# Kernel optimization log

Hardware: AMD Instinct MI355X
Metric: run time of the kernel (lower is better)

Reference implementation:

```python
import jax, jax.numpy as jnp
import numpy as np


def _hippo_dplr(n):
    # HiPPO-LegS -> NPLR -> DPLR (diagonal plus low rank) init, as in S4
    pr = np.sqrt(1.0 + 2.0 * np.arange(n))
    A = -(np.tril(pr[:, None] * pr[None, :]) - np.diag(np.arange(n)))
    p = np.sqrt(np.arange(n) + 0.5)
    b = np.sqrt(2.0 * np.arange(n) + 1.0)
    S = A + p[:, None] * p[None, :]
    lam_re = np.full(n, np.mean(np.diagonal(S)))
    lam_im, V = np.linalg.eigh(S * -1j)  # S*-1j is Hermitian
    p_c = V.conj().T @ p.astype(np.complex128)
    b_c = V.conj().T @ b.astype(np.complex128)
    return lam_re, lam_im, p_c, b_c


def setup_inputs():
    B, L, H, N = 4, 1024, 512, 64
    key = jax.random.key(0)
    kx, kc, ks, k1, k2 = jax.random.split(key, 5)
    lam_re, lam_im, p_c, b_c = _hippo_dplr(N)
    c = jax.random.normal(kc, (N, 2)) * (0.5 ** 0.5)
    f32 = lambda a: jnp.asarray(a, dtype=jnp.float32)
    return {
        'x': jax.random.normal(kx, (B, L, H), dtype=jnp.float32),
        'norm_weight': jnp.ones((H,), jnp.float32),
        'norm_bias': jnp.zeros((H,), jnp.float32),
        'lambda_re': f32(lam_re), 'lambda_im': f32(lam_im),
        'p_re': f32(p_c.real), 'p_im': f32(p_c.imag),
        'b_re': f32(b_c.real), 'b_im': f32(b_c.imag),
        'c_re': c[:, 0].astype(jnp.float32), 'c_im': c[:, 1].astype(jnp.float32),
        'd': jnp.ones((), jnp.float32),
        'log_step': jax.random.uniform(ks, (), jnp.float32, float(np.log(0.001)), float(np.log(0.1))),
        'out_w': (jax.random.normal(k1, (H, H), jnp.float32) / np.sqrt(H)).astype(jnp.float32),
        'out_b': jnp.zeros((H,), jnp.float32),
        'out2_w': (jax.random.normal(k2, (H, H), jnp.float32) / np.sqrt(H)).astype(jnp.float32),
        'out2_b': jnp.zeros((H,), jnp.float32),
    }


def reference(x, norm_weight, norm_bias, lambda_re, lambda_im, p_re, p_im,
              b_re, b_im, c_re, c_im, d, log_step, out_w, out_b, out2_w, out2_b):
    Bsz, L, H = x.shape
    skip = x
    # LayerNorm over channel dim (eps=1e-5, eqx default)
    mu = jnp.mean(x, -1, keepdims=True)
    var = jnp.mean((x - mu) ** 2, -1, keepdims=True)
    xn = (x - mu) / jnp.sqrt(var + 1e-5) * norm_weight + norm_bias
    # --- S4 DPLR bilinear discretization ---
    lam = (lambda_re + 1j * lambda_im).astype(jnp.complex64)
    p = (p_re + 1j * p_im).astype(jnp.complex64)
    b = (b_re + 1j * b_im).astype(jnp.complex64)
    c = (c_re + 1j * c_im).astype(jnp.complex64)
    step = jnp.exp(log_step).astype(jnp.complex64)
    N = lam.shape[0]
    I = jnp.eye(N, dtype=jnp.complex64)
    A = jnp.diag(lam) - p[:, None] * p[None, :].conj()
    A0 = (2.0 / step) * I + A
    Dinv = jnp.diag(1.0 / ((2.0 / step) - lam))
    qcD = p.conj()[None, :] @ Dinv           # [1,N]
    Dp = Dinv @ p[:, None]                   # [N,1]
    A1 = Dinv - (Dp @ qcD) / (1.0 + (qcD @ p[:, None]))  # Woodbury
    Ab = A1 @ A0                             # [N,N] discrete state matrix
    Bb = 2.0 * (A1 @ b[:, None])[:, 0]       # [N]
    # --- sequential state-space scan over time, vectorized over (B,H) lanes ---
    u = xn.astype(jnp.complex64)             # [B,L,H]

    def step_fn(state, u_t):                 # state: [B,H,N], u_t: [B,H]
        new = jnp.einsum('nm,bhm->bhn', Ab, state) + u_t[..., None] * Bb
        return new, jnp.einsum('n,bhn->bh', c, new).real

    init = jnp.zeros((Bsz, H, N), jnp.complex64)
    _, ys = jax.lax.scan(step_fn, init, jnp.moveaxis(u, 1, 0))  # ys: [L,B,H]
    y = jnp.moveaxis(ys, 0, 1) + d * xn      # feedthrough term
    # --- GELU + GLU-style gated output projection, residual ---
    y = jax.nn.gelu(y)
    gate = jax.nn.sigmoid(y @ out2_w.T + out2_b)
    return skip + (y @ out_w.T + out_b) * gate
```

## Files before the change

kernel.cpp:

```cpp
#include <hip/hip_runtime.h>
#include <math.h>

#define HDIM 512
#define LSEQ 1024
#define BSZ  4

typedef __attribute__((ext_vector_type(8))) short short8;
typedef __attribute__((ext_vector_type(4))) float floatx4;
typedef _Float16 half8 __attribute__((ext_vector_type(8)));

__device__ __forceinline__ float2 cmul(float2 a, float2 b) {
  float2 r;
  r.x = a.x * b.x - a.y * b.y;
  r.y = a.x * b.y + a.y * b.x;
  return r;
}
__device__ __forceinline__ float2 cadd(float2 a, float2 b) {
  float2 r; r.x = a.x + b.x; r.y = a.y + b.y; return r;
}
__device__ __forceinline__ float2 cfma(float2 a, float2 b, float2 c) {
  c.x += a.x * b.x - a.y * b.y;
  c.y += a.x * b.y + a.y * b.x;
  return c;
}
__device__ __forceinline__ ushort f2h(float f) {
  _Float16 h = (_Float16)f;
  return *(ushort*)&h;
}
__device__ __forceinline__ uint pack2h(float a, float b) {
  return (uint)f2h(a) | ((uint)f2h(b) << 16);
}

template<int CTRL, int RM>
__device__ __forceinline__ float dpp_add(float v) {
  int x = __builtin_amdgcn_update_dpp(0, __float_as_int(v), CTRL, RM, 0xF, false);
  return v + __int_as_float(x);
}
__device__ __forceinline__ float red8(float v) {
  v = dpp_add<0xB1, 0xF>(v);
  v = dpp_add<0x4E, 0xF>(v);
  v = dpp_add<0x141, 0xF>(v);
  return v;
}
__device__ __forceinline__ float red64(float v) {
  v = dpp_add<0x121, 0xF>(v);
  v = dpp_add<0x122, 0xF>(v);
  v = dpp_add<0x124, 0xF>(v);
  v = dpp_add<0x128, 0xF>(v);
  v = dpp_add<0x142, 0xA>(v);
  v = dpp_add<0x143, 0xC>(v);
  return __int_as_float(__builtin_amdgcn_readlane(__float_as_int(v), 63));
}

__global__ __launch_bounds__(576) void stage1_kernel(
    const float* __restrict__ x, const float* __restrict__ nw,
    const float* __restrict__ nb, ushort* __restrict__ xn16,
    const float* __restrict__ lre, const float* __restrict__ lim,
    const float* __restrict__ pre, const float* __restrict__ pim,
    const float* __restrict__ bre, const float* __restrict__ bim,
    const float* __restrict__ cre, const float* __restrict__ cim,
    const float* __restrict__ logstep, float* __restrict__ Kout,
    const float* __restrict__ w1, const float* __restrict__ w2,
    ushort* __restrict__ Wst) {
  __shared__ float2 Ldab[64], Lu[64], Lr[64], LBb[64];
  __shared__ float2 Rv[2048];
  __shared__ float2 Wv[2048];
  int tid = threadIdx.x;
  int wv = tid >> 6;
  int lane = tid & 63;

  if (blockIdx.x != 0) {
    int row = (blockIdx.x - 1) * 9 + wv;
    if (row < BSZ * LSEQ) {
      const float* xr = x + (size_t)row * HDIM;
      float4 v0 = ((const float4*)xr)[lane];
      float4 v1 = ((const float4*)xr)[lane + 64];
      float s  = v0.x + v0.y + v0.z + v0.w + v1.x + v1.y + v1.z + v1.w;
      float ss = v0.x*v0.x + v0.y*v0.y + v0.z*v0.z + v0.w*v0.w
               + v1.x*v1.x + v1.y*v1.y + v1.z*v1.z + v1.w*v1.w;
      s  = red64(s);
      ss = red64(ss);
      float mu   = s * (1.0f / HDIM);
      float var  = ss * (1.0f / HDIM) - mu * mu;
      float rstd = rsqrtf(var + 1e-5f);
      float4 w0 = ((const float4*)nw)[lane];
      float4 w1v = ((const float4*)nw)[lane + 64];
      float4 b0 = ((const float4*)nb)[lane];
      float4 b1 = ((const float4*)nb)[lane + 64];
      float4 o0, o1;
      o0.x = (v0.x - mu) * rstd * w0.x + b0.x;
      o0.y = (v0.y - mu) * rstd * w0.y + b0.y;
      o0.z = (v0.z - mu) * rstd * w0.z + b0.z;
      o0.w = (v0.w - mu) * rstd * w0.w + b0.w;
      o1.x = (v1.x - mu) * rstd * w1v.x + b1.x;
      o1.y = (v1.y - mu) * rstd * w1v.y + b1.y;
      o1.z = (v1.z - mu) * rstd * w1v.z + b1.z;
      o1.w = (v1.w - mu) * rstd * w1v.w + b1.w;
      ushort* xo = xn16 + (size_t)row * HDIM;
      uint2 p0, p1;
      p0.x = pack2h(o0.x, o0.y); p0.y = pack2h(o0.z, o0.w);
      p1.x = pack2h(o1.x, o1.y); p1.y = pack2h(o1.z, o1.w);
      *(uint2*)&xo[lane * 4]       = p0;
      *(uint2*)&xo[256 + lane * 4] = p1;
    }
    int idx = (blockIdx.x - 1) * 576 + tid;
    if (idx < 65536) {
      int e0 = idx * 8;
      int n = e0 >> 9, k0 = e0 & 511;
      const float* Wr = (n < 512) ? (w1 + (size_t)n * 512 + k0)
                                  : (w2 + (size_t)(n - 512) * 512 + k0);
      ushort tmp[8];
      #pragma unroll
      for (int q = 0; q < 8; q++) tmp[q] = f2h(Wr[q]);
      *(short8*)&Wst[e0] = *(short8*)tmp;
    }
    return;
  }

  if (tid < 64) {
    int n = tid;
    float step = expf(logstep[0]);
    float g = 2.0f / step;
    float lr = lre[n], li = lim[n];
    float pr = pre[n], pi = pim[n];
    float br = bre[n], bi = bim[n];
    float den  = (g - lr) * (g - lr) + li * li;
    float dinr = (g - lr) / den, dini = li / den;
    float dabr = (g + lr) * dinr - li * dini;
    float dabi = (g + lr) * dini + li * dinr;
    float ur = dinr * pr - dini * pi;
    float ui = dinr * pi + dini * pr;
    float qr = pr * dinr + pi * dini;
    float qi = pr * dini - pi * dinr;
    float pm2 = pr * pr + pi * pi;
    float betr = red64(pm2 * dinr);
    float beti = red64(pm2 * dini);
    float gar  = red64(qr * br - qi * bi);
    float gai  = red64(qr * bi + qi * br);
    float obr = 1.0f + betr, obi = beti;
    float ob2 = obr * obr + obi * obi;
    float kr = -2.0f * g * obr / ob2;
    float ki =  2.0f * g * obi / ob2;
    float rr = kr * qr - ki * qi;
    float ri = kr * qi + ki * qr;
    float tgr = (gar * obr + gai * obi) / ob2;
    float tgi = (gai * obr - gar * obi) / ob2;
    float dbr = dinr * br - dini * bi;
    float dbi = dinr * bi + dini * br;
    float Bbr = 2.0f * (dbr - (ur * tgr - ui * tgi));
    float Bbi = 2.0f * (dbi - (ur * tgi + ui * tgr));
    float2 t;
    t.x = dabr; t.y = dabi; Ldab[n] = t;
    t.x = ur;   t.y = ui;   Lu[n]   = t;
    t.x = rr;   t.y = ri;   Lr[n]   = t;
    t.x = Bbr;  t.y = Bbi;  LBb[n]  = t;
  }
  if (wv == 8) { float2 cc; cc.x = cre[lane]; cc.y = cim[lane]; Rv[lane] = cc; }
  __syncthreads();

  int g8 = lane >> 3;
  int q8 = lane & 7;
  int jm = wv * 8 + g8;
  float2 cv[8];

  if (wv < 8) {
    float2 dab[8], u[8], rn[8];
    #pragma unroll
    for (int ii = 0; ii < 8; ii++) {
      int n = q8 * 8 + ii;
      dab[ii] = Ldab[n]; u[ii] = Lu[n]; rn[ii] = Lr[n];
    }
    float2 rj = Lr[jm];
    #pragma unroll
    for (int ii = 0; ii < 8; ii++) {
      int n = q8 * 8 + ii;
      cv[ii] = cmul(u[ii], rj);
      if (n == jm) cv[ii] = cadd(cv[ii], dab[ii]);
    }
    for (int s = 0; s < 31; s++) {
      float2 part; part.x = 0.f; part.y = 0.f;
      #pragma unroll
      for (int ii = 0; ii < 8; ii++) part = cfma(rn[ii], cv[ii], part);
      part.x = red8(part.x);
      part.y = red8(part.y);
      #pragma unroll
      for (int ii = 0; ii < 8; ii++) {
        float2 nc = cmul(dab[ii], cv[ii]);
        cv[ii] = cfma(u[ii], part, nc);
      }
    }
  } else {
    float2 dab0 = Ldab[lane], u0 = Lu[lane], r0 = Lr[lane];
    float2 w = LBb[lane];
    Wv[lane * 32 + 0] = w;
    for (int b = 1; b < 32; b++) {
      float dr = red64(r0.x * w.x - r0.y * w.y);
      float di = red64(r0.x * w.y + r0.y * w.x);
      float2 nw2;
      nw2.x = dab0.x * w.x - dab0.y * w.y + u0.x * dr - u0.y * di;
      nw2.y = dab0.x * w.y + dab0.y * w.x + u0.x * di + u0.y * dr;
      w = nw2;
      Wv[lane * 32 + b] = w;
    }
  }
  __syncthreads();

  for (int a = 1; a < 32; a++) {
    if (wv < 8) {
      float2 part; part.x = 0.f; part.y = 0.f;
      #pragma unroll
      for (int ii = 0; ii < 8; ii++) {
        float2 Rk = Rv[(a - 1) * 64 + q8 * 8 + ii];
        part = cfma(Rk, cv[ii], part);
      }
      part.x = red8(part.x);
      part.y = red8(part.y);
      if (q8 == 0) Rv[a * 64 + jm] = part;
    }
    __syncthreads();
  }

  if (wv < 8) {
    int b = lane & 31, half = lane >> 5;
    #pragma unroll
    for (int a = 0; a < 4; a++) {
      int arow = wv * 4 + a;
      float acc = 0.f;
      #pragma unroll
      for (int n = 0; n < 32; n++) {
        float2 W = Wv[(half * 32 + n) * 32 + b];
        float2 R = Rv[arow * 64 + half * 32 + n];
        acc += R.x * W.x - R.y * W.y;
      }
      acc += __shfl_xor(acc, 32);
      if (half == 0) Kout[arow * 32 + b] = acc;
    }
  }
}

__global__ __launch_bounds__(256) void prep_kernel(
    const ushort* __restrict__ xn16, const float* __restrict__ K,
    ushort* __restrict__ Uhi, ushort* __restrict__ Thi) {
  __shared__ __attribute__((aligned(16))) ushort tile[64][72];
  int blk = blockIdx.x;
  int tid = threadIdx.x;
  if (blk < 512) {
    int ht = blk & 7, lt = (blk >> 3) & 15, b = blk >> 7;
    int r = tid >> 2;
    int sc = (tid & 3) * 16;
    const ushort* src = xn16 + ((size_t)(b * LSEQ + lt * 64 + r)) * HDIM + ht * 64 + sc;
    uint4 va = *(const uint4*)&src[0];
    uint4 vb = *(const uint4*)&src[8];
    *(uint4*)&tile[r][sc]     = va;
    *(uint4*)&tile[r][sc + 8] = vb;
    __syncthreads();
    int hr = tid >> 2;
    int c0 = (tid & 3) * 16;
    ushort tmp[16];
    #pragma unroll
    for (int q = 0; q < 16; q++) tmp[q] = tile[c0 + q][hr];
    ushort* dst = Uhi + ((size_t)(b * HDIM + ht * 64 + hr)) * LSEQ + lt * 64 + c0;
    *(uint4*)&dst[0] = *(uint4*)&tmp[0];
    *(uint4*)&dst[8] = *(uint4*)&tmp[8];
  } else {
    int r = blk - 512;
    int t = r * 2 + (tid >> 7);
    int tau0 = (tid & 127) * 8;
    int bound = ((t >> 6) + 1) << 6;
    if (tau0 < bound) {
      ushort hi[8];
      #pragma unroll
      for (int q = 0; q < 8; q++) {
        int tau = tau0 + q;
        float v = (tau <= t) ? K[t - tau] : 0.f;
        hi[q] = f2h(v);
      }
      *(short8*)&Thi[(size_t)t * 1024 + tau0] = *(short8*)hi;
    }
  }
}

__global__ __launch_bounds__(256) void conv_gemm_kernel(
    const ushort* __restrict__ Thi, const ushort* __restrict__ Uhi,
    const ushort* __restrict__ xn16, const float* __restrict__ dptr,
    ushort* __restrict__ A) {
  __shared__ __attribute__((aligned(16))) ushort sbuf[2 * 9216];
  int tid = threadIdx.x;
  int lane = tid & 63;
  int wv = tid >> 6;
  int wm = wv >> 1, wn = wv & 1;
  int by = blockIdx.y;
  int bm = (by < 8) ? by : 23 - by;
  int bn = blockIdx.x;
  floatx4 acc[2][2] = {};
  int srow = tid >> 2;
  int scol = (tid & 3) * 16;
  int ldst = srow * 72 + scol;
  int fr = lane & 15, fq = (lane >> 4) * 8;
  size_t Toff = (size_t)(bm * 64 + srow) * 1024 + scol;
  size_t Uoff = (size_t)(bn * 64 + srow) * 1024 + scol;
  int KT = bm + 1;
  uint4 t0 = *(const uint4*)&Thi[Toff];
  uint4 t1 = *(const uint4*)&Thi[Toff + 8];
  uint4 u0 = *(const uint4*)&Uhi[Uoff];
  uint4 u1 = *(const uint4*)&Uhi[Uoff + 8];
  *(uint4*)&sbuf[ldst]            = t0;
  *(uint4*)&sbuf[ldst + 8]        = t1;
  *(uint4*)&sbuf[ldst + 4608]     = u0;
  *(uint4*)&sbuf[ldst + 4608 + 8] = u1;
  __syncthreads();
  for (int kt = 0; kt < KT; kt++) {
    const ushort* src = sbuf + (kt & 1) * 9216;
    bool more = (kt + 1 < KT);
    if (more) {
      size_t k1 = (size_t)(kt + 1) * 64;
      t0 = *(const uint4*)&Thi[Toff + k1];
      t1 = *(const uint4*)&Thi[Toff + k1 + 8];
      u0 = *(const uint4*)&Uhi[Uoff + k1];
      u1 = *(const uint4*)&Uhi[Uoff + k1 + 8];
    }
    half8 ah[2][2], bh[2][2];
    #pragma unroll
    for (int i = 0; i < 2; i++) {
      int ar = (wm * 32 + i * 16 + fr) * 72;
      int br = 4608 + (wn * 32 + i * 16 + fr) * 72;
      ah[i][0] = *(const half8*)&src[ar + fq];
      ah[i][1] = *(const half8*)&src[ar + 32 + fq];
      bh[i][0] = *(const half8*)&src[br + fq];
      bh[i][1] = *(const half8*)&src[br + 32 + fq];
    }
    #pragma unroll
    for (int ks = 0; ks < 2; ks++)
      #pragma unroll
      for (int i = 0; i < 2; i++)
        #pragma unroll
        for (int j = 0; j < 2; j++)
          acc[i][j] = __builtin_amdgcn_mfma_f32_16x16x32_f16(ah[i][ks], bh[j][ks], acc[i][j], 0, 0, 0);
    if (more) {
      ushort* dst = sbuf + ((kt & 1) ^ 1) * 9216;
      *(uint4*)&dst[ldst]            = t0;
      *(uint4*)&dst[ldst + 8]        = t1;
      *(uint4*)&dst[ldst + 4608]     = u0;
      *(uint4*)&dst[ldst + 4608 + 8] = u1;
      __syncthreads();
    }
  }
  float d = dptr[0];
  int row0 = bm * 64 + wm * 32;
  int col0 = bn * 64 + wn * 32;
  int fc = lane & 15, frq = (lane >> 4) * 4;
  #pragma unroll
  for (int i = 0; i < 2; i++)
    #pragma unroll
    for (int j = 0; j < 2; j++)
      #pragma unroll
      for (int r = 0; r < 4; r++) {
        int t = row0 + i * 16 + frq + r;
        int c = col0 + j * 16 + fc;
        int b = c >> 9, h = c & 511;
        size_t off = (size_t)(b * LSEQ + t) * HDIM + h;
        float xv = (float)(*(const _Float16*)&xn16[off]);
        float y = acc[i][j][r] + d * xv;
        float z2 = 1.5957691216057308f * y * (1.0f + 0.044715f * y * y);
        float sg = __builtin_amdgcn_rcpf(1.0f + __expf(-z2));
        A[off] = f2h(y * sg);
      }
}

__global__ __launch_bounds__(256) void proj_kernel(
    const ushort* __restrict__ Abuf, const ushort* __restrict__ Wst,
    const float* __restrict__ x, const float* __restrict__ ob,
    const float* __restrict__ o2b, float* __restrict__ out) {
  __shared__ __attribute__((aligned(16))) ushort sbuf[2 * 13824];
  int tid = threadIdx.x;
  int lane = tid & 63;
  int wv = tid >> 6;
  int wm = wv >> 1, wn = wv & 1;
  int bm = blockIdx.y, bn = blockIdx.x;
  int srow = tid >> 2;
  int scol = (tid & 3) * 16;
  int ldst = srow * 72 + scol;
  int fr = lane & 15, fq = (lane >> 4) * 8;
  floatx4 acc1[2][2] = {}, acc2[2][2] = {};
  size_t Aoff  = (size_t)(bm * 64 + srow) * 512 + scol;
  size_t W1off = (size_t)(bn * 64 + srow) * 512 + scol;
  size_t W2off = W1off + (size_t)512 * 512;
  uint4 a0 = *(const uint4*)&Abuf[Aoff];
  uint4 a1 = *(const uint4*)&Abuf[Aoff + 8];
  uint4 v0 = *(const uint4*)&Wst[W1off];
  uint4 v1 = *(const uint4*)&Wst[W1off + 8];
  uint4 v2 = *(const uint4*)&Wst[W2off];
  uint4 v3 = *(const uint4*)&Wst[W2off + 8];
  *(uint4*)&sbuf[ldst]            = a0;
  *(uint4*)&sbuf[ldst + 8]        = a1;
  *(uint4*)&sbuf[ldst + 4608]     = v0;
  *(uint4*)&sbuf[ldst + 4608 + 8] = v1;
  *(uint4*)&sbuf[ldst + 9216]     = v2;
  *(uint4*)&sbuf[ldst + 9216 + 8] = v3;
  __syncthreads();
  for (int kt = 0; kt < 8; kt++) {
    const ushort* src = sbuf + (kt & 1) * 13824;
    bool more = (kt + 1 < 8);
    if (more) {
      int k1 = (kt + 1) * 64;
      a0 = *(const uint4*)&Abuf[Aoff + k1];
      a1 = *(const uint4*)&Abuf[Aoff + k1 + 8];
      v0 = *(const uint4*)&Wst[W1off + k1];
      v1 = *(const uint4*)&Wst[W1off + k1 + 8];
      v2 = *(const uint4*)&Wst[W2off + k1];
      v3 = *(const uint4*)&Wst[W2off + k1 + 8];
    }
    half8 af[2][2], b1[2][2], b2[2][2];
    #pragma unroll
    for (int i = 0; i < 2; i++) {
      int ar  = (wm * 32 + i * 16 + fr) * 72;
      int wr1 = 4608 + (wn * 32 + i * 16 + fr) * 72;
      int wr2 = 9216 + (wn * 32 + i * 16 + fr) * 72;
      af[i][0] = *(const half8*)&src[ar + fq];
      af[i][1] = *(const half8*)&src[ar + 32 + fq];
      b1[i][0] = *(const half8*)&src[wr1 + fq];
      b1[i][1] = *(const half8*)&src[wr1 + 32 + fq];
      b2[i][0] = *(const half8*)&src[wr2 + fq];
      b2[i][1] = *(const half8*)&src[wr2 + 32 + fq];
    }
    #pragma unroll
    for (int ks = 0; ks < 2; ks++)
      #pragma unroll
      for (int i = 0; i < 2; i++)
        #pragma unroll
        for (int j = 0; j < 2; j++) {
          acc1[i][j] = __builtin_amdgcn_mfma_f32_16x16x32_f16(af[i][ks], b1[j][ks], acc1[i][j], 0, 0, 0);
          acc2[i][j] = __builtin_amdgcn_mfma_f32_16x16x32_f16(af[i][ks], b2[j][ks], acc2[i][j], 0, 0, 0);
        }
    if (more) {
      ushort* dst = sbuf + ((kt & 1) ^ 1) * 13824;
      *(uint4*)&dst[ldst]            = a0;
      *(uint4*)&dst[ldst + 8]        = a1;
      *(uint4*)&dst[ldst + 4608]     = v0;
      *(uint4*)&dst[ldst + 4608 + 8] = v1;
      *(uint4*)&dst[ldst + 9216]     = v2;
      *(uint4*)&dst[ldst + 9216 + 8] = v3;
      __syncthreads();
    }
  }
  int row0 = bm * 64 + wm * 32;
  int col0 = bn * 64 + wn * 32;
  int fc = lane & 15, frq = (lane >> 4) * 4;
  #pragma unroll
  for (int i = 0; i < 2; i++)
    #pragma unroll
    for (int j = 0; j < 2; j++)
      #pragma unroll
      for (int r = 0; r < 4; r++) {
        int row = row0 + i * 16 + frq + r;
        int col = col0 + j * 16 + fc;
        float c1 = acc1[i][j][r] + ob[col];
        float c2 = acc2[i][j][r] + o2b[col];
        float gate = __builtin_amdgcn_rcpf(1.0f + __expf(-c2));
        size_t off = (size_t)row * HDIM + col;
        out[off] = x[off] + c1 * gate;
      }
}

extern "C" void kernel_launch(void* const* d_in, const int* in_sizes, int n_in,
                              void* d_out, int out_size, void* d_ws, size_t ws_size,
                              hipStream_t stream) {
  const float* x   = (const float*)d_in[0];
  const float* nw  = (const float*)d_in[1];
  const float* nb  = (const float*)d_in[2];
  const float* lre = (const float*)d_in[3];
  const float* lim = (const float*)d_in[4];
  const float* pre = (const float*)d_in[5];
  const float* pim = (const float*)d_in[6];
  const float* bre = (const float*)d_in[7];
  const float* bim = (const float*)d_in[8];
  const float* cre = (const float*)d_in[9];
  const float* cim = (const float*)d_in[10];
  const float* dsc = (const float*)d_in[11];
  const float* lst = (const float*)d_in[12];
  const float* w1  = (const float*)d_in[13];
  const float* ob  = (const float*)d_in[14];
  const float* w2  = (const float*)d_in[15];
  const float* o2b = (const float*)d_in[16];

  char* ws = (char*)d_ws;
  ushort* xn16 = (ushort*)(ws);
  ushort* Uhi  = (ushort*)(ws + (size_t)(8  << 20));
  ushort* Thi  = (ushort*)(ws + (size_t)(12 << 20));
  ushort* Wst  = (ushort*)(ws + (size_t)(16 << 20));
  ushort* Abuf = (ushort*)(ws + (size_t)(17 << 20));
  float* Kbuf  = (float*)(ws + (size_t)(21 << 20));
  float* out   = (float*)d_out;

  stage1_kernel<<<dim3(457), dim3(576), 0, stream>>>(x, nw, nb, xn16,
                                                     lre, lim, pre, pim, bre, bim,
                                                     cre, cim, lst, Kbuf,
                                                     w1, w2, Wst);
  prep_kernel<<<dim3(1024), dim3(256), 0, stream>>>(xn16, Kbuf, Uhi, Thi);
  conv_gemm_kernel<<<dim3(32, 16), dim3(256), 0, stream>>>(Thi, Uhi,
                                                           xn16, dsc, Abuf);
  proj_kernel<<<dim3(8, 64), dim3(256), 0, stream>>>(Abuf, Wst, x, ob, o2b, out);
}
```

Baseline: 147.4 us.

## Fuse transpose into layernorm stage and build Toeplitz tiles from kernel on the fly

Drops the separate prep kernel. The LayerNorm blocks now each handle a 64-row tile, stage it in shared memory and write the transposed Uhi layout directly. The conv GEMM builds its Toeplitz operand tiles from the short K vector at load time instead of reading a materialized Thi matrix, and a zeroed pad before K handles the causal mask. This saves one launch and the Thi write and read traffic. In exchange the stage1 grid shrinks to 65 blocks with large shared memory, which reduces parallelism, and the GEMM inner loop gains scalar gathers and fp16 packing.

```diff
diff --git a/kernel.cpp b/kernel.cpp
--- a/kernel.cpp
+++ b/kernel.cpp
@@ -59,53 +59,75 @@
     const float* __restrict__ pre, const float* __restrict__ pim,
     const float* __restrict__ bre, const float* __restrict__ bim,
     const float* __restrict__ cre, const float* __restrict__ cim,
-    const float* __restrict__ logstep, float* __restrict__ Kout,
+    const float* __restrict__ logstep, float* __restrict__ Kbuf,
     const float* __restrict__ w1, const float* __restrict__ w2,
-    ushort* __restrict__ Wst) {
+    ushort* __restrict__ Wst, ushort* __restrict__ Uhi) {
   __shared__ float2 Ldab[64], Lu[64], Lr[64], LBb[64];
   __shared__ float2 Rv[2048];
   __shared__ float2 Wv[2048];
+  __shared__ ushort tile[64][514];
   int tid = threadIdx.x;
   int wv = tid >> 6;
   int lane = tid & 63;
 
   if (blockIdx.x != 0) {
-    int row = (blockIdx.x - 1) * 9 + wv;
-    if (row < BSZ * LSEQ) {
-      const float* xr = x + (size_t)row * HDIM;
-      float4 v0 = ((const float4*)xr)[lane];
-      float4 v1 = ((const float4*)xr)[lane + 64];
-      float s  = v0.x + v0.y + v0.z + v0.w + v1.x + v1.y + v1.z + v1.w;
-      float ss = v0.x*v0.x + v0.y*v0.y + v0.z*v0.z + v0.w*v0.w
-               + v1.x*v1.x + v1.y*v1.y + v1.z*v1.z + v1.w*v1.w;
-      s  = red64(s);
-      ss = red64(ss);
-      float mu   = s * (1.0f / HDIM);
-      float var  = ss * (1.0f / HDIM) - mu * mu;
-      float rstd = rsqrtf(var + 1e-5f);
+    int s = blockIdx.x - 1;
+    int b = s >> 4, lt = s & 15;
+    if (wv < 8) {
       float4 w0 = ((const float4*)nw)[lane];
       float4 w1v = ((const float4*)nw)[lane + 64];
       float4 b0 = ((const float4*)nb)[lane];
       float4 b1 = ((const float4*)nb)[lane + 64];
-      float4 o0, o1;
-      o0.x = (v0.x - mu) * rstd * w0.x + b0.x;
-      o0.y = (v0.y - mu) * rstd * w0.y + b0.y;
-      o0.z = (v0.z - mu) * rstd * w0.z + b0.z;
-      o0.w = (v0.w - mu) * rstd * w0.w + b0.w;
-      o1.x = (v1.x - mu) * rstd * w1v.x + b1.x;
-      o1.y = (v1.y - mu) * rstd * w1v.y + b1.y;
-      o1.z = (v1.z - mu) * rstd * w1v.z + b1.z;
-      o1.w = (v1.w - mu) * rstd * w1v.w + b1.w;
-      ushort* xo = xn16 + (size_t)row * HDIM;
-      uint2 p0, p1;
-      p0.x = pack2h(o0.x, o0.y); p0.y = pack2h(o0.z, o0.w);
-      p1.x = pack2h(o1.x, o1.y); p1.y = pack2h(o1.z, o1.w);
-      *(uint2*)&xo[lane * 4]       = p0;
-      *(uint2*)&xo[256 + lane * 4] = p1;
-    }
-    int idx = (blockIdx.x - 1) * 576 + tid;
-    if (idx < 65536) {
-      int e0 = idx * 8;
+      #pragma unroll
+      for (int i = 0; i < 8; i++) {
+        int r = wv * 8 + i;
+        int row = b * LSEQ + lt * 64 + r;
+        const float* xr = x + (size_t)row * HDIM;
+        float4 v0 = ((const float4*)xr)[lane];
+        float4 v1 = ((const float4*)xr)[lane + 64];
+        float sm  = v0.x + v0.y + v0.z + v0.w + v1.x + v1.y + v1.z + v1.w;
+        float ssm = v0.x*v0.x + v0.y*v0.y + v0.z*v0.z + v0.w*v0.w
+                  + v1.x*v1.x + v1.y*v1.y + v1.z*v1.z + v1.w*v1.w;
+        sm  = red64(sm);
+        ssm = red64(ssm);
+        float mu   = sm * (1.0f / HDIM);
+        float var  = ssm * (1.0f / HDIM) - mu * mu;
+        float rstd = rsqrtf(var + 1e-5f);
+        float4 o0, o1;
+        o0.x = (v0.x - mu) * rstd * w0.x + b0.x;
+        o0.y = (v0.y - mu) * rstd * w0.y + b0.y;
+        o0.z = (v0.z - mu) * rstd * w0.z + b0.z;
+        o0.w = (v0.w - mu) * rstd * w0.w + b0.w;
+        o1.x = (v1.x - mu) * rstd * w1v.x + b1.x;
+        o1.y = (v1.y - mu) * rstd * w1v.y + b1.y;
+        o1.z = (v1.z - mu) * rstd * w1v.z + b1.z;
+        o1.w = (v1.w - mu) * rstd * w1v.w + b1.w;
+        uint2 p0, p1;
+        p0.x = pack2h(o0.x, o0.y); p0.y = pack2h(o0.z, o0.w);
+        p1.x = pack2h(o1.x, o1.y); p1.y = pack2h(o1.z, o1.w);
+        ushort* xo = xn16 + (size_t)row * HDIM;
+        *(uint2*)&xo[lane * 4]       = p0;
+        *(uint2*)&xo[256 + lane * 4] = p1;
+        *(uint*)&tile[r][lane * 4]           = p0.x;
+        *(uint*)&tile[r][lane * 4 + 2]       = p0.y;
+        *(uint*)&tile[r][256 + lane * 4]     = p1.x;
+        *(uint*)&tile[r][256 + lane * 4 + 2] = p1.y;
+      }
+    }
+    __syncthreads();
+    for (int t = tid; t < 2048; t += 576) {
+      int ht = t >> 8, rem = t & 255;
+      int hr = rem >> 2, c0 = (rem & 3) * 16;
+      int hcol = ht * 64 + hr;
+      ushort tmp[16];
+      #pragma unroll
+      for (int q = 0; q < 16; q++) tmp[q] = tile[c0 + q][hcol];
+      ushort* dst = Uhi + ((size_t)(b * HDIM + hcol)) * LSEQ + lt * 64 + c0;
+      *(uint4*)&dst[0] = *(uint4*)&tmp[0];
+      *(uint4*)&dst[8] = *(uint4*)&tmp[8];
+    }
+    for (int w = s * 576 + tid; w < 65536; w += 64 * 576) {
+      int e0 = w * 8;
       int n = e0 >> 9, k0 = e0 & 511;
       const float* Wr = (n < 512) ? (w1 + (size_t)n * 512 + k0)
                                   : (w2 + (size_t)(n - 512) * 512 + k0);
@@ -117,6 +139,7 @@
     return;
   }
 
+  if (tid < 64) Kbuf[tid] = 0.f;
   if (tid < 64) {
     int n = tid;
     float step = expf(logstep[0]);
@@ -233,58 +256,17 @@
         acc += R.x * W.x - R.y * W.y;
       }
       acc += __shfl_xor(acc, 32);
-      if (half == 0) Kout[arow * 32 + b] = acc;
-    }
-  }
-}
-
-__global__ __launch_bounds__(256) void prep_kernel(
-    const ushort* __restrict__ xn16, const float* __restrict__ K,
-    ushort* __restrict__ Uhi, ushort* __restrict__ Thi) {
-  __shared__ __attribute__((aligned(16))) ushort tile[64][72];
-  int blk = blockIdx.x;
-  int tid = threadIdx.x;
-  if (blk < 512) {
-    int ht = blk & 7, lt = (blk >> 3) & 15, b = blk >> 7;
-    int r = tid >> 2;
-    int sc = (tid & 3) * 16;
-    const ushort* src = xn16 + ((size_t)(b * LSEQ + lt * 64 + r)) * HDIM + ht * 64 + sc;
-    uint4 va = *(const uint4*)&src[0];
-    uint4 vb = *(const uint4*)&src[8];
-    *(uint4*)&tile[r][sc]     = va;
-    *(uint4*)&tile[r][sc + 8] = vb;
-    __syncthreads();
-    int hr = tid >> 2;
-    int c0 = (tid & 3) * 16;
-    ushort tmp[16];
-    #pragma unroll
-    for (int q = 0; q < 16; q++) tmp[q] = tile[c0 + q][hr];
-    ushort* dst = Uhi + ((size_t)(b * HDIM + ht * 64 + hr)) * LSEQ + lt * 64 + c0;
-    *(uint4*)&dst[0] = *(uint4*)&tmp[0];
-    *(uint4*)&dst[8] = *(uint4*)&tmp[8];
-  } else {
-    int r = blk - 512;
-    int t = r * 2 + (tid >> 7);
-    int tau0 = (tid & 127) * 8;
-    int bound = ((t >> 6) + 1) << 6;
-    if (tau0 < bound) {
-      ushort hi[8];
-      #pragma unroll
-      for (int q = 0; q < 8; q++) {
-        int tau = tau0 + q;
-        float v = (tau <= t) ? K[t - tau] : 0.f;
-        hi[q] = f2h(v);
-      }
-      *(short8*)&Thi[(size_t)t * 1024 + tau0] = *(short8*)hi;
+      if (half == 0) Kbuf[64 + arow * 32 + b] = acc;
     }
   }
 }
 
 __global__ __launch_bounds__(256) void conv_gemm_kernel(
-    const ushort* __restrict__ Thi, const ushort* __restrict__ Uhi,
-    const ushort* __restrict__ xn16, const float* __restrict__ dptr,
+    const ushort* __restrict__ Uhi, const ushort* __restrict__ xn16,
+    const float* __restrict__ Kbuf, const float* __restrict__ dptr,
     ushort* __restrict__ A) {
   __shared__ __attribute__((aligned(16))) ushort sbuf[2 * 9216];
+  const float* Kp = Kbuf + 64;
   int tid = threadIdx.x;
   int lane = tid & 63;
   int wv = tid >> 6;
@@ -296,26 +278,38 @@
   int srow = tid >> 2;
   int scol = (tid & 3) * 16;
   int ldst = srow * 72 + scol;
+  int trow = bm * 64 + srow;
   int fr = lane & 15, fq = (lane >> 4) * 8;
-  size_t Toff = (size_t)(bm * 64 + srow) * 1024 + scol;
   size_t Uoff = (size_t)(bn * 64 + srow) * 1024 + scol;
   int KT = bm + 1;
-  uint4 t0 = *(const uint4*)&Thi[Toff];
-  uint4 t1 = *(const uint4*)&Thi[Toff + 8];
+  float kva[16];
+  {
+    int base = trow - scol;
+    #pragma unroll
+    for (int q = 0; q < 16; q++) kva[q] = Kp[base - q];
+  }
   uint4 u0 = *(const uint4*)&Uhi[Uoff];
   uint4 u1 = *(const uint4*)&Uhi[Uoff + 8];
-  *(uint4*)&sbuf[ldst]            = t0;
-  *(uint4*)&sbuf[ldst + 8]        = t1;
-  *(uint4*)&sbuf[ldst + 4608]     = u0;
-  *(uint4*)&sbuf[ldst + 4608 + 8] = u1;
+  {
+    uint4 tw0, tw1;
+    tw0.x = pack2h(kva[0], kva[1]);   tw0.y = pack2h(kva[2], kva[3]);
+    tw0.z = pack2h(kva[4], kva[5]);   tw0.w = pack2h(kva[6], kva[7]);
+    tw1.x = pack2h(kva[8], kva[9]);   tw1.y = pack2h(kva[10], kva[11]);
+    tw1.z = pack2h(kva[12], kva[13]); tw1.w = pack2h(kva[14], kva[15]);
+    *(uint4*)&sbuf[ldst]            = tw0;
+    *(uint4*)&sbuf[ldst + 8]        = tw1;
+    *(uint4*)&sbuf[ldst + 4608]     = u0;
+    *(uint4*)&sbuf[ldst + 4608 + 8] = u1;
+  }
   __syncthreads();
   for (int kt = 0; kt < KT; kt++) {
     const ushort* src = sbuf + (kt & 1) * 9216;
     bool more = (kt + 1 < KT);
     if (more) {
+      int base = trow - (kt + 1) * 64 - scol;
+      #pragma unroll
+      for (int q = 0; q < 16; q++) kva[q] = Kp[base - q];
       size_t k1 = (size_t)(kt + 1) * 64;
-      t0 = *(const uint4*)&Thi[Toff + k1];
-      t1 = *(const uint4*)&Thi[Toff + k1 + 8];
       u0 = *(const uint4*)&Uhi[Uoff + k1];
       u1 = *(const uint4*)&Uhi[Uoff + k1 + 8];
     }
@@ -338,8 +332,13 @@
           acc[i][j] = __builtin_amdgcn_mfma_f32_16x16x32_f16(ah[i][ks], bh[j][ks], acc[i][j], 0, 0, 0);
     if (more) {
       ushort* dst = sbuf + ((kt & 1) ^ 1) * 9216;
-      *(uint4*)&dst[ldst]            = t0;
-      *(uint4*)&dst[ldst + 8]        = t1;
+      uint4 tw0, tw1;
+      tw0.x = pack2h(kva[0], kva[1]);   tw0.y = pack2h(kva[2], kva[3]);
+      tw0.z = pack2h(kva[4], kva[5]);   tw0.w = pack2h(kva[6], kva[7]);
+      tw1.x = pack2h(kva[8], kva[9]);   tw1.y = pack2h(kva[10], kva[11]);
+      tw1.z = pack2h(kva[12], kva[13]); tw1.w = pack2h(kva[14], kva[15]);
+      *(uint4*)&dst[ldst]            = tw0;
+      *(uint4*)&dst[ldst + 8]        = tw1;
       *(uint4*)&dst[ldst + 4608]     = u0;
       *(uint4*)&dst[ldst + 4608 + 8] = u1;
       __syncthreads();
@@ -486,18 +485,16 @@
   char* ws = (char*)d_ws;
   ushort* xn16 = (ushort*)(ws);
   ushort* Uhi  = (ushort*)(ws + (size_t)(8  << 20));
-  ushort* Thi  = (ushort*)(ws + (size_t)(12 << 20));
   ushort* Wst  = (ushort*)(ws + (size_t)(16 << 20));
   ushort* Abuf = (ushort*)(ws + (size_t)(17 << 20));
   float* Kbuf  = (float*)(ws + (size_t)(21 << 20));
   float* out   = (float*)d_out;
 
-  stage1_kernel<<<dim3(457), dim3(576), 0, stream>>>(x, nw, nb, xn16,
-                                                     lre, lim, pre, pim, bre, bim,
-                                                     cre, cim, lst, Kbuf,
-                                                     w1, w2, Wst);
-  prep_kernel<<<dim3(1024), dim3(256), 0, stream>>>(xn16, Kbuf, Uhi, Thi);
-  conv_gemm_kernel<<<dim3(32, 16), dim3(256), 0, stream>>>(Thi, Uhi,
-                                                           xn16, dsc, Abuf);
+  stage1_kernel<<<dim3(65), dim3(576), 0, stream>>>(x, nw, nb, xn16,
+                                                    lre, lim, pre, pim, bre, bim,
+                                                    cre, cim, lst, Kbuf,
+                                                    w1, w2, Wst, Uhi);
+  conv_gemm_kernel<<<dim3(32, 16), dim3(256), 0, stream>>>(Uhi, xn16, Kbuf,
+                                                           dsc, Abuf);
   proj_kernel<<<dim3(8, 64), dim3(256), 0, stream>>>(Abuf, Wst, x, ob, o2b, out);
 }
```

After: 152.1 us. 1.03x slower.
